# Kernel optimization log

Measured on AMD Instinct MI355X. Metric: run time of the kernel, lower is better.

The kernel has to match this reference:

```python
import jax, jax.numpy as jnp
import numpy as np

# Dimensions
B, NIN, P, K, D, F = 8, 4096, 1024, 16, 2, 64
CPF, C, DM = 64, 128, 2
CIN = CPF + F
BN_EPS = 1e-3  # Keras BatchNormalization default epsilon


def _bn(x, prm):
    # inference-mode batchnorm; prm is (4, C): gamma, beta, moving_mean, moving_var
    g, b, m, v = prm
    return g * (x - m) * jax.lax.rsqrt(v + BN_EPS) + b


def setup_inputs() -> dict:
    key = jax.random.key(0)
    ks = jax.random.split(key, 24)
    s = 0.05
    def rn(k, shape):
        return jax.random.normal(k, shape, jnp.float32) * s
    def bn_prm(k, c):
        kg, kb, km, kv = jax.random.split(k, 4)
        return jnp.stack([
            1.0 + 0.1 * jax.random.normal(kg, (c,), jnp.float32),
            0.1 * jax.random.normal(kb, (c,), jnp.float32),
            0.1 * jax.random.normal(km, (c,), jnp.float32),
            jax.random.uniform(kv, (c,), jnp.float32, 0.5, 1.5),
        ])
    inputs = jax.random.normal(ks[0], (B, NIN, 3 + F), jnp.float32)
    return {
        "inputs": inputs,
        "W_pf1": rn(ks[1], (3, CPF)), "b_pf1": rn(ks[2], (CPF,)), "bn_pf1": bn_prm(ks[3], CPF),
        "W_pf2": rn(ks[4], (CPF, CPF)), "b_pf2": rn(ks[5], (CPF,)), "bn_pf2": bn_prm(ks[6], CPF),
        "W_c1": rn(ks[7], (K, 3, K * K)), "b_c1": rn(ks[8], (K * K,)), "bn_c1": bn_prm(ks[9], K * K),
        "W_c2": rn(ks[10], (K, K, K)), "b_c2": rn(ks[11], (K * K,)), "bn_c2": bn_prm(ks[12], K * K),
        "W_c3": rn(ks[13], (K, K, K)), "b_c3": rn(ks[14], (K * K,)), "bn_c3": bn_prm(ks[15], K * K),
        "W_df": rn(ks[16], (K, CIN, DM)), "W_pw": rn(ks[17], (CIN * DM, C)),
        "b_f": rn(ks[18], (C,)), "bn_f": bn_prm(ks[19], C),
    }


def reference(inputs, W_pf1, b_pf1, bn_pf1, W_pf2, b_pf2, bn_pf2,
              W_c1, b_c1, bn_c1, W_c2, b_c2, bn_c2, W_c3, b_c3, bn_c3,
              W_df, W_pw, b_f, bn_f):
    p = inputs[:, :, :3]              # (B, NIN, 3) positions
    q = p[:, :P, :]                   # (B, P, 3) 'random' sampled query points
    # knn_indices_general(q, p, K*D, sorted=True): squared-distance top-k
    d2 = (q * q).sum(-1)[:, :, None] + (p * p).sum(-1)[:, None, :] \
         - 2.0 * jnp.einsum('bqc,bpc->bqp', q, p)          # (B, P, NIN)
    _, idx_kd = jax.lax.top_k(-d2, K * D)                  # ascending distance
    idx = idx_kd[:, :, ::D]                                # dilation -> (B, P, K)
    gathered = jnp.take_along_axis(
        inputs, idx.reshape(B, P * K)[:, :, None], axis=1).reshape(B, P, K, 3 + F)
    p_nb = gathered[..., :3] - q[:, :, None, :]            # (B, P, K, 3) local coords
    f_nb = gathered[..., 3:]                               # (B, P, K, F)
    # pos -> feature: Dense, BN, Dense, BN (no activation in source)
    h = _bn(p_nb @ W_pf1 + b_pf1, bn_pf1)
    h = _bn(h @ W_pf2 + b_pf2, bn_pf2)
    feat = jnp.concatenate([h, f_nb], axis=-1)             # (B, P, K, CIN)
    # Conv2D(K*K, (1,K), elu) + BN: contraction over neighbor axis
    x = _bn(jax.nn.elu(jnp.einsum('bnjc,jco->bno', p_nb, W_c1) + b_c1), bn_c1)
    x = x.reshape(B, P, K, K)
    # DepthwiseConv2D((1,K), mult=K, elu) + BN; Keras channel order c*mult+m
    x = _bn(jax.nn.elu(jnp.einsum('bnwc,wcm->bncm', x, W_c2).reshape(B, P, K * K) + b_c2), bn_c2)
    x = x.reshape(B, P, K, K)
    x = _bn(jax.nn.elu(jnp.einsum('bnwc,wcm->bncm', x, W_c3).reshape(B, P, K * K) + b_c3), bn_c3)
    x = x.reshape(B, P, K, K)
    # per-point KxK X-transform on gathered features
    feat = jnp.einsum('bnij,bnjc->bnic', x, feat)          # (B, P, K, CIN)
    # SeparableConv2D(C, (1,K), mult=DM, elu) + BN; width axis collapses
    dw = jnp.einsum('bnjc,jcm->bncm', feat, W_df).reshape(B, P, CIN * DM)
    out = _bn(jax.nn.elu(dw @ W_pw + b_f), bn_f)           # (B, P, C)
    return jnp.concatenate([q, out], axis=-1)              # (B, P, 3 + C)
```

## Files before the change

kernel.cpp:

```cpp
#include <hip/hip_runtime.h>
#include <math.h>

#define B_    8
#define NIN_  4096
#define P_    1024
#define K_    16
#define F_    64
#define CH_   67
#define CPF_  64
#define CIN_  128
#define C_    128

#define S_PF1  0
#define SH_PF1 64
#define S_PF2  128
#define SH_PF2 192
#define S_C1   256
#define SH_C1  512
#define S_C2   768
#define SH_C2  1024
#define S_C3   1280
#define SH_C3  1536
#define S_F    1792
#define SH_F   1920
#define M_OFF  2048
#define C0_OFF 2240

#define WS_PTS_OFF  16384
#define WS_DWL_OFF  (WS_PTS_OFF + B_ * NIN_ * 16)

typedef float f2 __attribute__((ext_vector_type(2)));
typedef float f4 __attribute__((ext_vector_type(4)));

__device__ __forceinline__ float rlf(float x, int l) {
    return __int_as_float(__builtin_amdgcn_readlane(__float_as_int(x), l));
}
__device__ __forceinline__ int rli(int x, int l) {
    return __builtin_amdgcn_readlane(x, l);
}
__device__ __forceinline__ float eluf(float z) {
    return z > 0.f ? z : (__expf(z) - 1.0f);
}
__device__ __forceinline__ float dpp_shr1_ninf(float x) {
    return __int_as_float(__builtin_amdgcn_update_dpp(
        (int)0xFF800000, __float_as_int(x), 0x138, 0xF, 0xF, false));
}
__device__ __forceinline__ int dpp_shr1_i(int x) {
    return __builtin_amdgcn_update_dpp(x, x, 0x138, 0xF, 0xF, false);
}

__global__ __launch_bounds__(256) void prep_kernel(
    const float* __restrict__ inp, float4* __restrict__ pts,
    const float* __restrict__ bn_pf1, const float* __restrict__ bn_pf2,
    const float* __restrict__ bn_c1,  const float* __restrict__ bn_c2,
    const float* __restrict__ bn_c3,  const float* __restrict__ bn_f,
    const float* __restrict__ Wpf1,   const float* __restrict__ bpf1,
    const float* __restrict__ Wpf2,   const float* __restrict__ bpf2,
    float* __restrict__ wsf) {
    const int tid = threadIdx.x;
    if (blockIdx.x < 128) {
        int i = blockIdx.x * 256 + tid;
        const float* r = inp + (size_t)i * CH_;
        float x = r[0], y = r[1], z = r[2];
        float pp = __fadd_rn(__fadd_rn(__fmul_rn(x, x), __fmul_rn(y, y)),
                             __fmul_rn(z, z));
        pts[i] = make_float4(x, y, z, __fmul_rn(0.5f, pp));
        return;
    }
#pragma unroll
    for (int it = 0; it < 4; ++it) {
        int t = it * 256 + tid;
        const float* src; int nch, c, so, sho;
        if (t < 64)       { src = bn_pf1; nch = 64;  c = t;        so = S_PF1; sho = SH_PF1; }
        else if (t < 128) { src = bn_pf2; nch = 64;  c = t - 64;   so = S_PF2; sho = SH_PF2; }
        else if (t < 384) { src = bn_c1;  nch = 256; c = t - 128;  so = S_C1;  sho = SH_C1; }
        else if (t < 640) { src = bn_c2;  nch = 256; c = t - 384;  so = S_C2;  sho = SH_C2; }
        else if (t < 896) { src = bn_c3;  nch = 256; c = t - 640;  so = S_C3;  sho = SH_C3; }
        else              { src = bn_f;   nch = 128; c = t - 896;  so = S_F;   sho = SH_F;  }
        float g = src[c], b = src[nch + c], m = src[2 * nch + c], v = src[3 * nch + c];
        float s = g * rsqrtf(v + 1e-3f);
        wsf[so + c]  = s;
        wsf[sho + c] = b - m * s;
    }
    __syncthreads();
    {
        __shared__ float4 red[4][64];
        const int o = tid & 63, part = tid >> 6;
        float m0 = 0.f, m1 = 0.f, m2 = 0.f, cc = 0.f;
        for (int c = part * 16; c < part * 16 + 16; ++c) {
            float s1 = wsf[S_PF1 + c], t1 = wsf[SH_PF1 + c];
            float d1 = s1 * bpf1[c] + t1;
            float w2 = Wpf2[c * 64 + o];
            m0 += Wpf1[0 * 64 + c] * s1 * w2;
            m1 += Wpf1[1 * 64 + c] * s1 * w2;
            m2 += Wpf1[2 * 64 + c] * s1 * w2;
            cc += d1 * w2;
        }
        red[part][o] = make_float4(m0, m1, m2, cc);
        __syncthreads();
        if (part == 0) {
            float4 p0 = red[0][o], p1 = red[1][o], p2 = red[2][o], p3 = red[3][o];
            float M0 = ((p0.x + p1.x) + p2.x) + p3.x;
            float M1 = ((p0.y + p1.y) + p2.y) + p3.y;
            float M2 = ((p0.z + p1.z) + p2.z) + p3.z;
            float CC = ((p0.w + p1.w) + p2.w) + p3.w;
            float s2 = wsf[S_PF2 + o], t2 = wsf[SH_PF2 + o];
            wsf[M_OFF + 0 * 64 + o] = M0 * s2;
            wsf[M_OFF + 1 * 64 + o] = M1 * s2;
            wsf[M_OFF + 2 * 64 + o] = M2 * s2;
            wsf[C0_OFF + o]         = CC * s2 + bpf2[o] * s2 + t2;
        }
    }
}

__global__ __launch_bounds__(256) void fused_kernel(
    const float4* __restrict__ pts, const float* __restrict__ inp,
    const float* __restrict__ Wc1,  const float* __restrict__ bc1,
    const float* __restrict__ Wc2,  const float* __restrict__ bc2,
    const float* __restrict__ Wc3,  const float* __restrict__ bc3,
    const float* __restrict__ Wdf,  const float* __restrict__ wsf,
    float* __restrict__ dwl, float* __restrict__ out) {

    __shared__ float xA[4][256];
    __shared__ float xB[4][256];

    const int w   = threadIdx.x >> 6;
    const int l   = threadIdx.x & 63;
    const int wid = (blockIdx.x << 2) | w;
    const int b   = wid >> 10;
    const int qi  = wid & 1023;
    const float4* bp = pts + ((size_t)b << 12);

    const float4 q = bp[qi];
    const float hq = q.w;

#define DIST2(P) __fsub_rn(__fadd_rn(hq, (P).w), \
    __fadd_rn(__fadd_rn(__fmul_rn(q.x, (P).x), __fmul_rn(q.y, (P).y)), \
              __fmul_rn(q.z, (P).z)))

    float4 p  = bp[l];
    float4 g1 = bp[64 + l];
    float4 g2 = bp[128 + l];
    float4 g3 = bp[192 + l];

    float d = DIST2(p);
    int ii = l;
#pragma unroll
    for (int k = 2; k <= 64; k <<= 1) {
#pragma unroll
        for (int j = k >> 1; j > 0; j >>= 1) {
            float od = __shfl_xor(d, j);
            int   oi = __shfl_xor(ii, j);
            bool keepmin = (((l & k) == 0) == ((l & j) == 0));
            bool ol = (od < d) || (od == d && oi < ii);
            bool take = keepmin ? ol : !ol;
            if (take) { d = od; ii = oi; }
        }
    }
    float bd = d;
    int   bi = ii;
    float kth = rlf(bd, 31);

#define INS_LOOP(MV, D2V, BASE)                                        \
    if (MV) {                                                          \
        do {                                                           \
            int c = (int)__builtin_ctzll(MV); MV &= MV - 1;            \
            float dc = rlf(D2V, c);                                    \
            int   ic = (BASE) + c;                                     \
            float prev  = dpp_shr1_ninf(bd);                           \
            int   previ = dpp_shr1_i(bi);                              \
            bool c1 = (bd > dc);                                       \
            bool c2 = (prev > dc);                                     \
            bd = fminf(bd, fmaxf(prev, dc));                           \
            bi = c1 ? (c2 ? previ : ic) : bi;                          \
        } while (MV);                                                  \
        kth = rlf(bd, 31);                                             \
    }

    {
        float d2 = DIST2(g1);
        unsigned long long m = __ballot(d2 < kth);
        INS_LOOP(m, d2, 64);
    }
    for (int j0 = 128; j0 < NIN_; j0 += 128) {
        float4 pa = g2, pb = g3;
        int jn = j0 + 128;
        if (jn < NIN_) { g2 = bp[jn + l]; g3 = bp[jn + 64 + l]; }
        float d2a = DIST2(pa);
        unsigned long long ma = __ballot(d2a < kth);
        INS_LOOP(ma, d2a, j0);
        float d2b = DIST2(pb);
        unsigned long long mb = __ballot(d2b < kth);
        INS_LOOP(mb, d2b, j0 + 64);
    }
#undef INS_LOOP
#undef DIST2

    const float* brow = inp + (size_t)b * NIN_ * CH_;
    const float q0 = q.x, q1 = q.y, q2 = q.z;

    float pd;
    {
        int k3 = (l * 21846) >> 16;
        k3 = (k3 > 15) ? 15 : k3;
        int d3 = l - ((k3 << 1) + k3);
        d3 = (d3 > 2) ? 2 : d3;
        int nbl = __shfl(bi, k3 << 1);
        float v = 0.f;
        if (l < 48) v = brow[(size_t)nbl * CH_ + d3];
        float qv = (d3 == 0) ? q0 : ((d3 == 1) ? q1 : q2);
        pd = v - qv;
    }

    {
        f4 acc = *reinterpret_cast<const f4*>(bc1 + 4 * l);
#pragma unroll 4
        for (int t4 = 0; t4 < 12; ++t4) {
            const float* wb = Wc1 + (size_t)(t4 * 4) * 256 + 4 * l;
            f4 w0 = *reinterpret_cast<const f4*>(wb);
            f4 w1 = *reinterpret_cast<const f4*>(wb + 256);
            f4 w2 = *reinterpret_cast<const f4*>(wb + 512);
            f4 w3 = *reinterpret_cast<const f4*>(wb + 768);
            float p0 = rlf(pd, 4 * t4 + 0);
            float p1 = rlf(pd, 4 * t4 + 1);
            float p2 = rlf(pd, 4 * t4 + 2);
            float p3 = rlf(pd, 4 * t4 + 3);
            acc += p0 * w0 + p1 * w1 + p2 * w2 + p3 * w3;
        }
        f4 sc = *reinterpret_cast<const f4*>(wsf + S_C1 + 4 * l);
        f4 sh = *reinterpret_cast<const f4*>(wsf + SH_C1 + 4 * l);
        f4 r;
        r.x = sc.x * eluf(acc.x) + sh.x;
        r.y = sc.y * eluf(acc.y) + sh.y;
        r.z = sc.z * eluf(acc.z) + sh.z;
        r.w = sc.w * eluf(acc.w) + sh.w;
        *reinterpret_cast<f4*>(&xA[w][4 * l]) = r;
    }

    {
        f4 acc = *reinterpret_cast<const f4*>(bc2 + 4 * l);
        const int csel = l >> 2;
#pragma unroll 8
        for (int w16 = 0; w16 < 16; ++w16) {
            float xs = xA[w][w16 * 16 + csel];
            f4 w4 = *reinterpret_cast<const f4*>(Wc2 + (size_t)w16 * 256 + 4 * l);
            acc += xs * w4;
        }
        f4 sc = *reinterpret_cast<const f4*>(wsf + S_C2 + 4 * l);
        f4 sh = *reinterpret_cast<const f4*>(wsf + SH_C2 + 4 * l);
        f4 r;
        r.x = sc.x * eluf(acc.x) + sh.x;
        r.y = sc.y * eluf(acc.y) + sh.y;
        r.z = sc.z * eluf(acc.z) + sh.z;
        r.w = sc.w * eluf(acc.w) + sh.w;
        *reinterpret_cast<f4*>(&xB[w][4 * l]) = r;
    }

    {
        f4 acc = *reinterpret_cast<const f4*>(bc3 + 4 * l);
        const int csel = l >> 2;
#pragma unroll 8
        for (int w16 = 0; w16 < 16; ++w16) {
            float xs = xB[w][w16 * 16 + csel];
            f4 w4 = *reinterpret_cast<const f4*>(Wc3 + (size_t)w16 * 256 + 4 * l);
            acc += xs * w4;
        }
        f4 sc = *reinterpret_cast<const f4*>(wsf + S_C3 + 4 * l);
        f4 sh = *reinterpret_cast<const f4*>(wsf + SH_C3 + 4 * l);
        f4 r;
        r.x = sc.x * eluf(acc.x) + sh.x;
        r.y = sc.y * eluf(acc.y) + sh.y;
        r.z = sc.z * eluf(acc.z) + sh.z;
        r.w = sc.w * eluf(acc.w) + sh.w;
        *reinterpret_cast<f4*>(&xA[w][4 * l]) = r;
    }

    f2 hf[16];
    {
        const float Mw0 = wsf[M_OFF + l];
        const float Mw1 = wsf[M_OFF + 64 + l];
        const float Mw2 = wsf[M_OFF + 128 + l];
        const float cc0 = wsf[C0_OFF + l];
#pragma unroll
        for (int k = 0; k < 16; ++k) {
            int nbs = rli(bi, 2 * k);
            float fv = brow[(size_t)nbs * CH_ + 3 + l];
            float s0 = rlf(pd, 3 * k), s1 = rlf(pd, 3 * k + 1), s2 = rlf(pd, 3 * k + 2);
            float hv = fmaf(s0, Mw0, fmaf(s1, Mw1, fmaf(s2, Mw2, cc0)));
            f2 t; t.x = hv; t.y = fv;
            hf[k] = t;
        }
    }

    f2 dlo; dlo.x = 0.f; dlo.y = 0.f;
    f2 dhi = dlo;
#pragma unroll 4
    for (int i = 0; i < 16; ++i) {
        const f4* xr = reinterpret_cast<const f4*>(&xA[w][i * 16]);
        f4 x0 = xr[0], x1 = xr[1], x2 = xr[2], x3v = xr[3];
        f2 fab = x0.x * hf[0]  + x0.y * hf[1]  + x0.z * hf[2]  + x0.w * hf[3]
               + x1.x * hf[4]  + x1.y * hf[5]  + x1.z * hf[6]  + x1.w * hf[7]
               + x2.x * hf[8]  + x2.y * hf[9]  + x2.z * hf[10] + x2.w * hf[11]
               + x3v.x * hf[12]+ x3v.y * hf[13]+ x3v.z * hf[14]+ x3v.w * hf[15];
        const float* wr = Wdf + (size_t)i * 256;
        f2 wlo = *reinterpret_cast<const f2*>(wr + 2 * l);
        f2 whi = *reinterpret_cast<const f2*>(wr + 128 + 2 * l);
        dlo += fab.x * wlo;
        dhi += fab.y * whi;
    }
    float* drow = dwl + (size_t)wid * 256;
    *reinterpret_cast<f2*>(drow + 2 * l)       = dlo;
    *reinterpret_cast<f2*>(drow + 128 + 2 * l) = dhi;

    if (l < 3) out[(size_t)wid * 131 + l] = (l == 0) ? q0 : ((l == 1) ? q1 : q2);
}

__global__ __launch_bounds__(256) void pw_kernel(const float* __restrict__ dwl,
                                                 const float* __restrict__ Wpw,
                                                 const float* __restrict__ bf,
                                                 const float* __restrict__ wsf,
                                                 float* __restrict__ out) {
    __shared__ float As[16][256];
    const int tid = threadIdx.x;
    const int m0  = blockIdx.x * 16;

#pragma unroll
    for (int i = 0; i < 4; ++i) {
        int fi  = i * 1024 + tid * 4;
        int row = fi >> 8, col = fi & 255;
        *reinterpret_cast<float4*>(&As[row][col]) =
            *reinterpret_cast<const float4*>(dwl + (size_t)(m0 + row) * 256 + col);
    }
    __syncthreads();

    const int mq = tid >> 5;
    const int nq = tid & 31;
    f4 acc[2];
#pragma unroll
    for (int mi = 0; mi < 2; ++mi) { acc[mi].x = 0.f; acc[mi].y = 0.f; acc[mi].z = 0.f; acc[mi].w = 0.f; }

#pragma unroll 4
    for (int k4 = 0; k4 < 64; ++k4) {
        f4 a[2], bw[4];
#pragma unroll
        for (int mi = 0; mi < 2; ++mi)
            a[mi] = *reinterpret_cast<const f4*>(&As[mq * 2 + mi][k4 * 4]);
#pragma unroll
        for (int ki = 0; ki < 4; ++ki)
            bw[ki] = *reinterpret_cast<const f4*>(Wpw + (size_t)(k4 * 4 + ki) * 128 + nq * 4);
#pragma unroll
        for (int mi = 0; mi < 2; ++mi) {
            acc[mi] += a[mi].x * bw[0] + a[mi].y * bw[1] + a[mi].z * bw[2] + a[mi].w * bw[3];
        }
    }

    f4 b4  = *reinterpret_cast<const f4*>(bf + nq * 4);
    f4 sc4 = *reinterpret_cast<const f4*>(wsf + S_F + nq * 4);
    f4 sh4 = *reinterpret_cast<const f4*>(wsf + SH_F + nq * 4);
#pragma unroll
    for (int mi = 0; mi < 2; ++mi) {
        const int m = m0 + mq * 2 + mi;
        float* orow = out + (size_t)m * 131 + 3 + nq * 4;
        orow[0] = sc4.x * eluf(acc[mi].x + b4.x) + sh4.x;
        orow[1] = sc4.y * eluf(acc[mi].y + b4.y) + sh4.y;
        orow[2] = sc4.z * eluf(acc[mi].z + b4.z) + sh4.z;
        orow[3] = sc4.w * eluf(acc[mi].w + b4.w) + sh4.w;
    }
}

extern "C" void kernel_launch(void* const* d_in, const int* in_sizes, int n_in,
                              void* d_out, int out_size, void* d_ws, size_t ws_size,
                              hipStream_t stream) {
    const float* inp   = (const float*)d_in[0];
    const float* Wpf1  = (const float*)d_in[1];
    const float* bpf1  = (const float*)d_in[2];
    const float* bnpf1 = (const float*)d_in[3];
    const float* Wpf2  = (const float*)d_in[4];
    const float* bpf2  = (const float*)d_in[5];
    const float* bnpf2 = (const float*)d_in[6];
    const float* Wc1   = (const float*)d_in[7];
    const float* bc1   = (const float*)d_in[8];
    const float* bnc1  = (const float*)d_in[9];
    const float* Wc2   = (const float*)d_in[10];
    const float* bc2   = (const float*)d_in[11];
    const float* bnc2  = (const float*)d_in[12];
    const float* Wc3   = (const float*)d_in[13];
    const float* bc3   = (const float*)d_in[14];
    const float* bnc3  = (const float*)d_in[15];
    const float* Wdf   = (const float*)d_in[16];
    const float* Wpw   = (const float*)d_in[17];
    const float* bf    = (const float*)d_in[18];
    const float* bnf   = (const float*)d_in[19];

    float*  wsf  = (float*)d_ws;
    float4* pts  = (float4*)((char*)d_ws + WS_PTS_OFF);
    float*  dwl  = (float*)((char*)d_ws + WS_DWL_OFF);
    float*  outp = (float*)d_out;

    hipLaunchKernelGGL(prep_kernel, dim3(129), dim3(256), 0, stream,
                       inp, pts, bnpf1, bnpf2, bnc1, bnc2, bnc3, bnf,
                       Wpf1, bpf1, Wpf2, bpf2, wsf);
    hipLaunchKernelGGL(fused_kernel, dim3((B_ * P_) / 4), dim3(256), 0, stream,
                       pts, inp, Wc1, bc1, Wc2, bc2, Wc3, bc3, Wdf, wsf,
                       dwl, outp);
    hipLaunchKernelGGL(pw_kernel, dim3((B_ * P_) / 16), dim3(256), 0, stream,
                       dwl, Wpw, bf, wsf, outp);
}
```

Measured before the change: 107.0 us.

## Fuse pointwise conv GEMM into main kernel and drop separate pw kernel

Moves the pointwise Dense (CIN*DM→C) plus bias, ELU and BN epilogue into the fused per-point kernel, staging each wave's depthwise output in shared memory instead of writing it to a workspace buffer. This removes one kernel launch and the global round trip of the intermediate. In exchange, each wave streams the full pointwise weight matrix itself, losing the multi-row weight reuse the separate tiled GEMM had.

```diff
diff --git a/kernel.cpp b/kernel.cpp
--- a/kernel.cpp
+++ b/kernel.cpp
@@ -27,7 +27,6 @@
 #define C0_OFF 2240
 
 #define WS_PTS_OFF  16384
-#define WS_DWL_OFF  (WS_PTS_OFF + B_ * NIN_ * 16)
 
 typedef float f2 __attribute__((ext_vector_type(2)));
 typedef float f4 __attribute__((ext_vector_type(4)));
@@ -118,8 +117,9 @@
     const float* __restrict__ Wc1,  const float* __restrict__ bc1,
     const float* __restrict__ Wc2,  const float* __restrict__ bc2,
     const float* __restrict__ Wc3,  const float* __restrict__ bc3,
-    const float* __restrict__ Wdf,  const float* __restrict__ wsf,
-    float* __restrict__ dwl, float* __restrict__ out) {
+    const float* __restrict__ Wdf,  const float* __restrict__ Wpw,
+    const float* __restrict__ bf,   const float* __restrict__ wsf,
+    float* __restrict__ out) {
 
     __shared__ float xA[4][256];
     __shared__ float xB[4][256];
@@ -308,64 +308,32 @@
         dlo += fab.x * wlo;
         dhi += fab.y * whi;
     }
-    float* drow = dwl + (size_t)wid * 256;
-    *reinterpret_cast<f2*>(drow + 2 * l)       = dlo;
-    *reinterpret_cast<f2*>(drow + 128 + 2 * l) = dhi;
-
-    if (l < 3) out[(size_t)wid * 131 + l] = (l == 0) ? q0 : ((l == 1) ? q1 : q2);
-}
-
-__global__ __launch_bounds__(256) void pw_kernel(const float* __restrict__ dwl,
-                                                 const float* __restrict__ Wpw,
-                                                 const float* __restrict__ bf,
-                                                 const float* __restrict__ wsf,
-                                                 float* __restrict__ out) {
-    __shared__ float As[16][256];
-    const int tid = threadIdx.x;
-    const int m0  = blockIdx.x * 16;
-
-#pragma unroll
-    for (int i = 0; i < 4; ++i) {
-        int fi  = i * 1024 + tid * 4;
-        int row = fi >> 8, col = fi & 255;
-        *reinterpret_cast<float4*>(&As[row][col]) =
-            *reinterpret_cast<const float4*>(dwl + (size_t)(m0 + row) * 256 + col);
-    }
-    __syncthreads();
-
-    const int mq = tid >> 5;
-    const int nq = tid & 31;
-    f4 acc[2];
-#pragma unroll
-    for (int mi = 0; mi < 2; ++mi) { acc[mi].x = 0.f; acc[mi].y = 0.f; acc[mi].z = 0.f; acc[mi].w = 0.f; }
-
-#pragma unroll 4
+
+    *reinterpret_cast<f2*>(&xA[w][2 * l])       = dlo;
+    *reinterpret_cast<f2*>(&xA[w][128 + 2 * l]) = dhi;
+
+    f2 o;
+    o.x = bf[2 * l];
+    o.y = bf[2 * l + 1];
+#pragma unroll 8
     for (int k4 = 0; k4 < 64; ++k4) {
-        f4 a[2], bw[4];
-#pragma unroll
-        for (int mi = 0; mi < 2; ++mi)
-            a[mi] = *reinterpret_cast<const f4*>(&As[mq * 2 + mi][k4 * 4]);
-#pragma unroll
-        for (int ki = 0; ki < 4; ++ki)
-            bw[ki] = *reinterpret_cast<const f4*>(Wpw + (size_t)(k4 * 4 + ki) * 128 + nq * 4);
-#pragma unroll
-        for (int mi = 0; mi < 2; ++mi) {
-            acc[mi] += a[mi].x * bw[0] + a[mi].y * bw[1] + a[mi].z * bw[2] + a[mi].w * bw[3];
-        }
-    }
-
-    f4 b4  = *reinterpret_cast<const f4*>(bf + nq * 4);
-    f4 sc4 = *reinterpret_cast<const f4*>(wsf + S_F + nq * 4);
-    f4 sh4 = *reinterpret_cast<const f4*>(wsf + SH_F + nq * 4);
-#pragma unroll
-    for (int mi = 0; mi < 2; ++mi) {
-        const int m = m0 + mq * 2 + mi;
-        float* orow = out + (size_t)m * 131 + 3 + nq * 4;
-        orow[0] = sc4.x * eluf(acc[mi].x + b4.x) + sh4.x;
-        orow[1] = sc4.y * eluf(acc[mi].y + b4.y) + sh4.y;
-        orow[2] = sc4.z * eluf(acc[mi].z + b4.z) + sh4.z;
-        orow[3] = sc4.w * eluf(acc[mi].w + b4.w) + sh4.w;
-    }
+        f4 dv = *reinterpret_cast<const f4*>(&xA[w][4 * k4]);
+        const float* wp = Wpw + (size_t)(4 * k4) * 128 + 2 * l;
+        f2 w0 = *reinterpret_cast<const f2*>(wp);
+        f2 w1 = *reinterpret_cast<const f2*>(wp + 128);
+        f2 w2 = *reinterpret_cast<const f2*>(wp + 256);
+        f2 w3 = *reinterpret_cast<const f2*>(wp + 384);
+        o += dv.x * w0 + dv.y * w1 + dv.z * w2 + dv.w * w3;
+    }
+    f2 sc = *reinterpret_cast<const f2*>(wsf + S_F + 2 * l);
+    f2 sh = *reinterpret_cast<const f2*>(wsf + SH_F + 2 * l);
+    f2 res;
+    res.x = sc.x * eluf(o.x) + sh.x;
+    res.y = sc.y * eluf(o.y) + sh.y;
+
+    float* orow = out + (size_t)wid * 131;
+    *reinterpret_cast<f2*>(orow + 3 + 2 * l) = res;
+    if (l < 3) orow[l] = (l == 0) ? q0 : ((l == 1) ? q1 : q2);
 }
 
 extern "C" void kernel_launch(void* const* d_in, const int* in_sizes, int n_in,
@@ -394,15 +362,12 @@
 
     float*  wsf  = (float*)d_ws;
     float4* pts  = (float4*)((char*)d_ws + WS_PTS_OFF);
-    float*  dwl  = (float*)((char*)d_ws + WS_DWL_OFF);
     float*  outp = (float*)d_out;
 
     hipLaunchKernelGGL(prep_kernel, dim3(129), dim3(256), 0, stream,
                        inp, pts, bnpf1, bnpf2, bnc1, bnc2, bnc3, bnf,
                        Wpf1, bpf1, Wpf2, bpf2, wsf);
     hipLaunchKernelGGL(fused_kernel, dim3((B_ * P_) / 4), dim3(256), 0, stream,
-                       pts, inp, Wc1, bc1, Wc2, bc2, Wc3, bc3, Wdf, wsf,
-                       dwl, outp);
-    hipLaunchKernelGGL(pw_kernel, dim3((B_ * P_) / 16), dim3(256), 0, stream,
-                       dwl, Wpw, bf, wsf, outp);
-}
+                       pts, inp, Wc1, bc1, Wc2, bc2, Wc3, bc3, Wdf, Wpw,
+                       bf, wsf, outp);
+}
```

Result: slower. 131.1 us (+22.5%).
